# Kernel tuning notes

Measured on AMD Instinct MI355X. Metric: run time of the kernel, lower is better.

The kernel has to match this reference:

```python
import jax, jax.numpy as jnp
import numpy as np

# Module hyperparameters (from init_kwargs)
DT_W = 0.1
TAU_W = 10.0
ALPHA_W = DT_W / TAU_W                      # 0.01
SIGMA_W = float(np.sqrt(2.0 / ALPHA_W) * 0.01)  # sqrt(2/alpha) * sigma_w
WEIGHT_BOUND = 1.0
B, OUT, IN = 64, 1024, 1024


def setup_inputs() -> dict:
    key = jax.random.key(0)
    k_w, k_b, k_pre, k_post, k_kappa, k_noise = jax.random.split(key, 6)
    return {
        "w": jax.random.uniform(k_w, (B, OUT, IN), dtype=jnp.float32),
        "baseline": jax.random.uniform(k_b, (OUT, IN), dtype=jnp.float32),
        "R": jnp.ones((B, 1, 1), dtype=jnp.float32),
        "pre": jax.random.uniform(k_pre, (B, IN), dtype=jnp.float32),
        "post": jax.random.uniform(k_post, (B, OUT), dtype=jnp.float32),
        "kappa": jax.random.uniform(k_kappa, (OUT, IN), dtype=jnp.float32),
        "noise": jax.random.normal(k_noise, (B, OUT, IN), dtype=jnp.float32),
    }


def reference(w, baseline, R, pre, post, kappa, noise):
    # hebb[b,o,i] = post[b,o] * pre[b,i]  (rank-1 outer product per batch)
    hebb = jnp.einsum("bo,bi->boi", post, pre)
    eff_lr = jnp.abs(kappa)                      # plas_mask is None
    new_w = (baseline * ALPHA_W
             + w * (1.0 - ALPHA_W)
             + R * eff_lr * (hebb + SIGMA_W * noise))
    # clamp to [lb, ub] = [0, weight_bound]
    return jnp.clip(new_w, 0.0, WEIGHT_BOUND)
```

## Files before the change

kernel.cpp:

```cpp
#include <hip/hip_runtime.h>


constexpr int B_DIM  = 64;
constexpr int OUT_D  = 1024;
constexpr int IN_D   = 1024;
constexpr int IN4    = IN_D / 4;
constexpr int TOTAL4 = B_DIM * OUT_D * IN4;
constexpr int BLOCK  = 256;
constexpr int GRID   = 2048;
constexpr int NTH    = BLOCK * GRID;
constexpr int ITERS  = TOTAL4 / NTH;

constexpr float ALPHA  = 0.01f;
constexpr float ONE_MA = 1.0f - ALPHA;
constexpr float SIGMA  = 0.14142135623730951f;

typedef float f32x4 __attribute__((ext_vector_type(4)));

__global__ __launch_bounds__(BLOCK)
void PlasticSynapse_69466801045994_kernel(
    const float4* __restrict__ w,
    const float4* __restrict__ baseline,
    const float*  __restrict__ R,
    const float4* __restrict__ pre,
    const float*  __restrict__ post,
    const float4* __restrict__ kappa,
    const float4* __restrict__ noise,
    float4*       __restrict__ out)
{
    const int tid = blockIdx.x * BLOCK + threadIdx.x;

    const int i4  = tid & (IN4 - 1);
    const int bo0 = tid >> 8;
    const int o   = bo0 & (OUT_D - 1);
    const int b0  = bo0 >> 10;
    const int oi  = o * IN4 + i4;

    const float4 bl = baseline[oi];
    const float4 kp = kappa[oi];
    float4 blA, ak;
    blA.x = bl.x * ALPHA;  blA.y = bl.y * ALPHA;
    blA.z = bl.z * ALPHA;  blA.w = bl.w * ALPHA;
    ak.x  = fabsf(kp.x);   ak.y  = fabsf(kp.y);
    ak.z  = fabsf(kp.z);   ak.w  = fabsf(kp.w);

#pragma unroll 4
    for (int k = 0; k < ITERS; ++k) {
        const int idx = tid + k * NTH;
        const int b   = b0 + 2 * k;

        const float4 wv = w[idx];
        const float4 nv = noise[idx];
        const float4 pr = pre[b * IN4 + i4];
        const float  po = post[b * OUT_D + o];
        const float  r  = R[b];

        const float lrx = r * ak.x;
        const float lry = r * ak.y;
        const float lrz = r * ak.z;
        const float lrw = r * ak.w;

        float4 res;
        res.x = fminf(fmaxf(fmaf(lrx, fmaf(SIGMA, nv.x, po * pr.x),
                                 fmaf(wv.x, ONE_MA, blA.x)), 0.0f), 1.0f);
        res.y = fminf(fmaxf(fmaf(lry, fmaf(SIGMA, nv.y, po * pr.y),
                                 fmaf(wv.y, ONE_MA, blA.y)), 0.0f), 1.0f);
        res.z = fminf(fmaxf(fmaf(lrz, fmaf(SIGMA, nv.z, po * pr.z),
                                 fmaf(wv.z, ONE_MA, blA.z)), 0.0f), 1.0f);
        res.w = fminf(fmaxf(fmaf(lrw, fmaf(SIGMA, nv.w, po * pr.w),
                                 fmaf(wv.w, ONE_MA, blA.w)), 0.0f), 1.0f);

        __builtin_nontemporal_store(*(const f32x4*)&res, (f32x4*)&out[idx]);
    }
}

extern "C" void kernel_launch(void* const* d_in, const int* in_sizes, int n_in,
                              void* d_out, int out_size, void* d_ws, size_t ws_size,
                              hipStream_t stream) {
    const float4* w        = (const float4*)d_in[0];
    const float4* baseline = (const float4*)d_in[1];
    const float*  R        = (const float*) d_in[2];
    const float4* pre      = (const float4*)d_in[3];
    const float*  post     = (const float*) d_in[4];
    const float4* kappa    = (const float4*)d_in[5];
    const float4* noise    = (const float4*)d_in[6];
    float4*       out      = (float4*)d_out;

    PlasticSynapse_69466801045994_kernel<<<GRID, BLOCK, 0, stream>>>(
        w, baseline, R, pre, post, kappa, noise, out);
}
```

Measured before the change: 586.4 us.

## Map blocks to (row, batch-half) with register-prefetched batch loop

Each block now handles one output row and half the batch, walking 32 batch slices with one-step software prefetch of w/noise/pre/post/R into registers. It also drops the nontemporal store in favour of a normal store and adds an occupancy hint to launch_bounds. The aim is more memory-level parallelism per thread and simpler indexing. The cost is a serialized dependent loop with only one load in flight per stream, and output writes may now pollute the cache.

```diff
diff --git a/kernel.cpp b/kernel.cpp
--- a/kernel.cpp
+++ b/kernel.cpp
@@ -5,19 +5,34 @@
 constexpr int OUT_D  = 1024;
 constexpr int IN_D   = 1024;
 constexpr int IN4    = IN_D / 4;
-constexpr int TOTAL4 = B_DIM * OUT_D * IN4;
 constexpr int BLOCK  = 256;
-constexpr int GRID   = 2048;
-constexpr int NTH    = BLOCK * GRID;
-constexpr int ITERS  = TOTAL4 / NTH;
+constexpr int BSPLIT = 2;
+constexpr int BITER  = B_DIM / BSPLIT;
+constexpr int GRID   = OUT_D * BSPLIT;
+constexpr int STEP   = OUT_D * IN4;
 
 constexpr float ALPHA  = 0.01f;
 constexpr float ONE_MA = 1.0f - ALPHA;
 constexpr float SIGMA  = 0.14142135623730951f;
 
-typedef float f32x4 __attribute__((ext_vector_type(4)));
+__device__ __forceinline__ float4 upd(const float4 wv, const float4 nv,
+                                      const float4 pr, const float po,
+                                      const float r,
+                                      const float4 ak, const float4 blA)
+{
+    float4 res;
+    res.x = fminf(fmaxf(fmaf(r * ak.x, fmaf(SIGMA, nv.x, po * pr.x),
+                             fmaf(wv.x, ONE_MA, blA.x)), 0.0f), 1.0f);
+    res.y = fminf(fmaxf(fmaf(r * ak.y, fmaf(SIGMA, nv.y, po * pr.y),
+                             fmaf(wv.y, ONE_MA, blA.y)), 0.0f), 1.0f);
+    res.z = fminf(fmaxf(fmaf(r * ak.z, fmaf(SIGMA, nv.z, po * pr.z),
+                             fmaf(wv.z, ONE_MA, blA.z)), 0.0f), 1.0f);
+    res.w = fminf(fmaxf(fmaf(r * ak.w, fmaf(SIGMA, nv.w, po * pr.w),
+                             fmaf(wv.w, ONE_MA, blA.w)), 0.0f), 1.0f);
+    return res;
+}
 
-__global__ __launch_bounds__(BLOCK)
+__global__ __launch_bounds__(BLOCK, 8)
 void PlasticSynapse_69466801045994_kernel(
     const float4* __restrict__ w,
     const float4* __restrict__ baseline,
@@ -28,49 +43,43 @@
     const float4* __restrict__ noise,
     float4*       __restrict__ out)
 {
-    const int tid = blockIdx.x * BLOCK + threadIdx.x;
+    const int o    = (int)blockIdx.x >> 1;
+    const int bh   = (int)blockIdx.x & 1;
+    const int i4   = (int)threadIdx.x;
+    const int b0   = bh * BITER;
+    const int bend = b0 + BITER;
 
-    const int i4  = tid & (IN4 - 1);
-    const int bo0 = tid >> 8;
-    const int o   = bo0 & (OUT_D - 1);
-    const int b0  = bo0 >> 10;
-    const int oi  = o * IN4 + i4;
-
+    const int oi = o * IN4 + i4;
     const float4 bl = baseline[oi];
     const float4 kp = kappa[oi];
-    float4 blA, ak;
-    blA.x = bl.x * ALPHA;  blA.y = bl.y * ALPHA;
-    blA.z = bl.z * ALPHA;  blA.w = bl.w * ALPHA;
-    ak.x  = fabsf(kp.x);   ak.y  = fabsf(kp.y);
-    ak.z  = fabsf(kp.z);   ak.w  = fabsf(kp.w);
+    float4 ak, blA;
+    ak.x  = fabsf(kp.x);  ak.y  = fabsf(kp.y);
+    ak.z  = fabsf(kp.z);  ak.w  = fabsf(kp.w);
+    blA.x = bl.x * ALPHA; blA.y = bl.y * ALPHA;
+    blA.z = bl.z * ALPHA; blA.w = bl.w * ALPHA;
 
-#pragma unroll 4
-    for (int k = 0; k < ITERS; ++k) {
-        const int idx = tid + k * NTH;
-        const int b   = b0 + 2 * k;
+    int idxC = (b0 * OUT_D + o) * IN4 + i4;
 
-        const float4 wv = w[idx];
-        const float4 nv = noise[idx];
-        const float4 pr = pre[b * IN4 + i4];
-        const float  po = post[b * OUT_D + o];
-        const float  r  = R[b];
+    float4 wC  = w[idxC];
+    float4 nC  = noise[idxC];
+    float4 pC  = pre[b0 * IN4 + i4];
+    float  poC = post[b0 * OUT_D + o];
+    float  rC  = R[b0];
 
-        const float lrx = r * ak.x;
-        const float lry = r * ak.y;
-        const float lrz = r * ak.z;
-        const float lrw = r * ak.w;
+    for (int b = b0; b < bend; ++b) {
+        const bool last = (b + 1 >= bend);
+        const int  bn   = last ? b : b + 1;
+        const int  idxN = idxC + (last ? 0 : STEP);
 
-        float4 res;
-        res.x = fminf(fmaxf(fmaf(lrx, fmaf(SIGMA, nv.x, po * pr.x),
-                                 fmaf(wv.x, ONE_MA, blA.x)), 0.0f), 1.0f);
-        res.y = fminf(fmaxf(fmaf(lry, fmaf(SIGMA, nv.y, po * pr.y),
-                                 fmaf(wv.y, ONE_MA, blA.y)), 0.0f), 1.0f);
-        res.z = fminf(fmaxf(fmaf(lrz, fmaf(SIGMA, nv.z, po * pr.z),
-                                 fmaf(wv.z, ONE_MA, blA.z)), 0.0f), 1.0f);
-        res.w = fminf(fmaxf(fmaf(lrw, fmaf(SIGMA, nv.w, po * pr.w),
-                                 fmaf(wv.w, ONE_MA, blA.w)), 0.0f), 1.0f);
+        const float4 wN  = w[idxN];
+        const float4 nN  = noise[idxN];
+        const float4 pN  = pre[bn * IN4 + i4];
+        const float  poN = post[bn * OUT_D + o];
+        const float  rN  = R[bn];
 
-        __builtin_nontemporal_store(*(const f32x4*)&res, (f32x4*)&out[idx]);
+        out[idxC] = upd(wC, nC, pC, poC, rC, ak, blA);
+
+        wC = wN; nC = nN; pC = pN; poC = poN; rC = rN; idxC = idxN;
     }
 }
 
```

Result: no change. 594.1 us (+1.3%).
